# Kernel tuning notes

Measured on AMD Instinct MI355X. Metric: run time of the kernel, lower is better.

## Reference

```python
import jax, jax.numpy as jnp
import numpy as np

ALPHA = 0.5  # leak rate (module default)


def setup_inputs() -> dict:
    key = jax.random.key(0)
    k1, k2, k3 = jax.random.split(key, 3)
    T, nInput, nRes = 4096, 4096, 2048
    x = jax.random.normal(k1, (T, nInput), dtype=jnp.float32)
    # gamma=0.01 scaled input weights, as in the module
    Win = 0.01 * jax.random.normal(k2, (nInput, nRes), dtype=jnp.float32)
    # recurrent weights ~ unit spectral radius (1/sqrt(N) scaling of iid gaussian)
    W = jax.random.normal(k3, (nRes, nRes), dtype=jnp.float32) / jnp.sqrt(nRes)
    return {"x": x, "Win": Win, "W": W}


def reference(x, Win, W):
    # Input projection is time-independent -> hoist out of the recurrence.
    uproj = x @ Win  # [T, nRes]

    def step(v, u):
        v_new = (1.0 - ALPHA) * v + ALPHA * jnp.tanh(v @ W + u)
        return v_new, v_new

    v0 = jnp.zeros((W.shape[0],), dtype=x.dtype)
    _, states = jax.lax.scan(step, v0, uproj)  # states: [T, nRes]
    return states
```

## Files before the change

kernel.cpp:

```cpp
#include <hip/hip_runtime.h>

#define NRES 2048
#define NBLK 256
#define RBUF 4

typedef unsigned long long u64;

__global__ __launch_bounds__(256) void transpose_k(const float* __restrict__ W,
                                                   float* __restrict__ Wt) {
  __shared__ float tile[32][33];
  const int tx = threadIdx.x, ty = threadIdx.y;
  const int x = blockIdx.x * 32 + tx;
  const int y0 = blockIdx.y * 32;
#pragma unroll
  for (int j = ty; j < 32; j += 8)
    tile[j][tx] = W[(size_t)(y0 + j) * NRES + x];
  __syncthreads();
  const int x2 = blockIdx.y * 32 + tx;
  const int y2 = blockIdx.x * 32;
#pragma unroll
  for (int j = ty; j < 32; j += 8)
    Wt[(size_t)(y2 + j) * NRES + x2] = tile[tx][j];
}

__global__ __launch_bounds__(256) void gemm_uproj(const float* __restrict__ X,
                                                  const float* __restrict__ B,
                                                  float* __restrict__ U,
                                                  int M, int N, int K) {
  __shared__ float As[16][128];
  __shared__ float Bs[16][128];
  const int tid = threadIdx.x;
  const int tx = tid & 15, ty = tid >> 4;
  const int m0 = blockIdx.y * 128, n0 = blockIdx.x * 128;

  float acc[8][8];
#pragma unroll
  for (int i = 0; i < 8; i++)
#pragma unroll
    for (int j = 0; j < 8; j++) acc[i][j] = 0.f;

  const int sam = tid >> 1, sak = (tid & 1) * 8;
  const int sbk = tid >> 4, sbn = (tid & 15) * 8;

  for (int k0 = 0; k0 < K; k0 += 16) {
    const float* ap = X + (size_t)(m0 + sam) * K + k0 + sak;
    float4 a0 = *(const float4*)(ap);
    float4 a1 = *(const float4*)(ap + 4);
    As[sak + 0][sam] = a0.x; As[sak + 1][sam] = a0.y;
    As[sak + 2][sam] = a0.z; As[sak + 3][sam] = a0.w;
    As[sak + 4][sam] = a1.x; As[sak + 5][sam] = a1.y;
    As[sak + 6][sam] = a1.z; As[sak + 7][sam] = a1.w;
    const float* bp = B + (size_t)(k0 + sbk) * N + n0 + sbn;
    *(float4*)&Bs[sbk][sbn]     = *(const float4*)(bp);
    *(float4*)&Bs[sbk][sbn + 4] = *(const float4*)(bp + 4);
    __syncthreads();
#pragma unroll
    for (int kk = 0; kk < 16; kk++) {
      float a[8], b[8];
      *(float4*)&a[0] = *(const float4*)&As[kk][ty * 8];
      *(float4*)&a[4] = *(const float4*)&As[kk][ty * 8 + 4];
      *(float4*)&b[0] = *(const float4*)&Bs[kk][tx * 8];
      *(float4*)&b[4] = *(const float4*)&Bs[kk][tx * 8 + 4];
#pragma unroll
      for (int i = 0; i < 8; i++)
#pragma unroll
        for (int j = 0; j < 8; j++) acc[i][j] += a[i] * b[j];
    }
    __syncthreads();
  }
#pragma unroll
  for (int i = 0; i < 8; i++) {
    float* dst = U + (size_t)(m0 + ty * 8 + i) * N + n0 + tx * 8;
    *(float4*)dst       = *(float4*)&acc[i][0];
    *(float4*)(dst + 4) = *(float4*)&acc[i][4];
  }
}

__global__ __launch_bounds__(256, 1) void esn_scan(const float* __restrict__ Wt,
                                                   const float* __restrict__ W,
                                                   u64* vtag,
                                                   float* __restrict__ UY,
                                                   int T) {
  __shared__ float v_lds[2][NRES];
  const int b = blockIdx.x;
  const int tid = threadIdx.x;
  const int wv = tid >> 6;
  const int lane = tid & 63;
  const int h = lane >> 5;
  const int s = lane & 31;
  const int j = b * 8 + wv * 2 + h;

  float2 w2[32];
  if (Wt) {
    const float2* wrow = (const float2*)(Wt + (size_t)j * NRES);
#pragma unroll
    for (int k = 0; k < 32; ++k) w2[k] = wrow[s + 32 * k];
  } else {
#pragma unroll
    for (int k = 0; k < 32; ++k) {
      w2[k].x = W[(size_t)(2 * s + 64 * k) * NRES + j];
      w2[k].y = W[(size_t)(2 * s + 64 * k + 1) * NRES + j];
    }
  }

  float vold = 0.f;

#pragma unroll
  for (int q = 0; q < 8; ++q) v_lds[0][tid + 256 * q] = 0.f;
  __syncthreads();

  for (int t = 0; t < T; ++t) {
    const int buf = t & 1;
    const size_t idx = (size_t)t * NRES + j;
    float u = (s == 0) ? UY[idx] : 0.f;

    if (t > 0) {
      u64* src = vtag + (size_t)((t - 1) & (RBUF - 1)) * NRES;
      unsigned done = 0;
      while (done != 0xFFu) {
        u64 w[8];
#pragma unroll
        for (int q = 0; q < 8; ++q)
          w[q] = __hip_atomic_load(&src[tid + 256 * q], __ATOMIC_RELAXED,
                                   __HIP_MEMORY_SCOPE_AGENT);
#pragma unroll
        for (int q = 0; q < 8; ++q) {
          if (!(done & (1u << q)) && (unsigned)(w[q] >> 32) == (unsigned)t) {
            v_lds[buf][tid + 256 * q] = __uint_as_float((unsigned)w[q]);
            done |= 1u << q;
          }
        }
      }
      __syncthreads();
    }

    float acc0 = 0.f, acc1 = 0.f;
#pragma unroll
    for (int k = 0; k < 32; k += 2) {
      float2 va = *(const float2*)&v_lds[buf][2 * s + 64 * k];
      float2 vb = *(const float2*)&v_lds[buf][2 * s + 64 * (k + 1)];
      acc0 += w2[k].x * va.x + w2[k].y * va.y;
      acc1 += w2[k + 1].x * vb.x + w2[k + 1].y * vb.y;
    }
    float acc = acc0 + acc1;
#pragma unroll
    for (int off = 16; off >= 1; off >>= 1) acc += __shfl_xor(acc, off);

    if (s == 0) {
      float xx = acc + u;
      float e = __expf(2.f * xx);
      float th = 1.f - 2.f / (e + 1.f);
      float vnew = 0.5f * vold + 0.5f * th;
      vold = vnew;
      UY[idx] = vnew;
      u64 w = ((u64)(unsigned)(t + 1) << 32) | (u64)__float_as_uint(vnew);
      (void)__hip_atomic_exchange(&vtag[(size_t)(t & (RBUF - 1)) * NRES + j],
                                  w, __ATOMIC_RELAXED,
                                  __HIP_MEMORY_SCOPE_AGENT);
    }
  }
}

extern "C" void kernel_launch(void* const* d_in, const int* in_sizes, int n_in,
                              void* d_out, int out_size, void* d_ws, size_t ws_size,
                              hipStream_t stream) {
  const float* x   = (const float*)d_in[0];
  const float* Win = (const float*)d_in[1];
  const float* W   = (const float*)d_in[2];
  float* U = (float*)d_out;

  const int T = out_size / NRES;
  const int K = in_sizes[0] / T;

  char* ws = (char*)d_ws;
  u64* vtag = (u64*)ws;
  const size_t vtag_bytes = (size_t)RBUF * NRES * sizeof(u64);
  float* Wt = nullptr;
  const size_t wt_need = vtag_bytes + (size_t)NRES * NRES * sizeof(float);
  if (ws_size >= wt_need) Wt = (float*)(ws + vtag_bytes);

  hipMemsetAsync(vtag, 0, vtag_bytes, stream);

  if (Wt) transpose_k<<<dim3(NRES / 32, NRES / 32), dim3(32, 8), 0, stream>>>(W, Wt);

  gemm_uproj<<<dim3(NRES / 128, T / 128), 256, 0, stream>>>(x, Win, U, T, NRES, K);

  void* args[] = {(void*)&Wt, (void*)&W, (void*)&vtag, (void*)&U, (void*)&T};
  hipLaunchCooperativeKernel((const void*)esn_scan, dim3(NBLK), dim3(256), args,
                             0, stream);
}
```

Before: 14.29 ms.

## Relay recurrent state through per-XCD mirror buffers to cut cross-die polling

Elects one block per XCD (read from the XCC_ID hardware register) as a relay. Only that block polls the global tagged state buffer, and it copies each value it observes into a mirror buffer belonging to its XCD. The other blocks first spin on their local mirror with sc0 loads, which are meant to hit the XCD-local L2, and fall back to global polling after a bounded number of spins. The aim is to cut cross-die coherence traffic and poll latency in the per-step grid sync. In exchange it adds an extra hop of latency through the relay, and it depends on the relay block making progress.

After: 30.01 ms. +110.0%, slower.

```diff
diff --git a/kernel.cpp b/kernel.cpp
--- a/kernel.cpp
+++ b/kernel.cpp
@@ -3,8 +3,11 @@
 #define NRES 2048
 #define NBLK 256
 #define RBUF 4
+#define NXCD 8
+#define MIR_SPINS 16
 
 typedef unsigned long long u64;
+typedef unsigned int u32;
 
 __global__ __launch_bounds__(256) void transpose_k(const float* __restrict__ W,
                                                    float* __restrict__ Wt) {
@@ -79,9 +82,12 @@
 __global__ __launch_bounds__(256, 1) void esn_scan(const float* __restrict__ Wt,
                                                    const float* __restrict__ W,
                                                    u64* vtag,
+                                                   u64* mirror,
+                                                   u32* xcd_cnt,
                                                    float* __restrict__ UY,
-                                                   int T) {
+                                                   int T, int relay_on) {
   __shared__ float v_lds[2][NRES];
+  __shared__ int sh_relay, sh_xcd;
   const int b = blockIdx.x;
   const int tid = threadIdx.x;
   const int wv = tid >> 6;
@@ -90,6 +96,15 @@
   const int s = lane & 31;
   const int j = b * 8 + wv * 2 + h;
 
+  if (tid == 0) {
+    u32 xcc;
+    asm volatile("s_getreg_b32 %0, hwreg(HW_REG_XCC_ID)" : "=s"(xcc));
+    const int mx = (int)(xcc & (NXCD - 1));
+    sh_xcd = mx;
+    int rank = relay_on ? (int)atomicAdd(&xcd_cnt[mx * 16], 1u) : 1;
+    sh_relay = (relay_on && rank == 0) ? 1 : 0;
+  }
+
   float2 w2[32];
   if (Wt) {
     const float2* wrow = (const float2*)(Wt + (size_t)j * NRES);
@@ -104,10 +119,11 @@
   }
 
   float vold = 0.f;
-
 #pragma unroll
   for (int q = 0; q < 8; ++q) v_lds[0][tid + 256 * q] = 0.f;
   __syncthreads();
+  const int myxcd = sh_xcd;
+  const bool polls_global = (sh_relay != 0) || !relay_on;
 
   for (int t = 0; t < T; ++t) {
     const int buf = t & 1;
@@ -115,19 +131,69 @@
     float u = (s == 0) ? UY[idx] : 0.f;
 
     if (t > 0) {
-      u64* src = vtag + (size_t)((t - 1) & (RBUF - 1)) * NRES;
+      const int slot = (t - 1) & (RBUF - 1);
+      u64* src = vtag + (size_t)slot * NRES;
       unsigned done = 0;
-      while (done != 0xFFu) {
-        u64 w[8];
-#pragma unroll
-        for (int q = 0; q < 8; ++q)
-          w[q] = __hip_atomic_load(&src[tid + 256 * q], __ATOMIC_RELAXED,
-                                   __HIP_MEMORY_SCOPE_AGENT);
-#pragma unroll
-        for (int q = 0; q < 8; ++q) {
-          if (!(done & (1u << q)) && (unsigned)(w[q] >> 32) == (unsigned)t) {
-            v_lds[buf][tid + 256 * q] = __uint_as_float((unsigned)w[q]);
-            done |= 1u << q;
+      if (polls_global) {
+        u64* mir = mirror + ((size_t)myxcd * RBUF + slot) * NRES;
+        while (done != 0xFFu) {
+          u64 w[8];
+#pragma unroll
+          for (int q = 0; q < 8; ++q)
+            w[q] = __hip_atomic_load(&src[tid + 256 * q], __ATOMIC_RELAXED,
+                                     __HIP_MEMORY_SCOPE_AGENT);
+#pragma unroll
+          for (int q = 0; q < 8; ++q) {
+            if (!(done & (1u << q)) && (u32)(w[q] >> 32) == (u32)t) {
+              if (relay_on) mir[tid + 256 * q] = w[q];
+              v_lds[buf][tid + 256 * q] = __uint_as_float((u32)w[q]);
+              done |= 1u << q;
+            }
+          }
+        }
+      } else {
+        const u64 mb =
+            (u64)(mirror + ((size_t)myxcd * RBUF + slot) * NRES) + (u64)tid * 8u;
+        for (int spin = 0; done != 0xFFu && spin < MIR_SPINS; ++spin) {
+          u64 w0, w1, w2_, w3, w4, w5, w6, w7;
+          asm volatile(
+              "global_load_dwordx2 %0, %8, off sc0\n\t"
+              "global_load_dwordx2 %1, %9, off sc0\n\t"
+              "global_load_dwordx2 %2, %10, off sc0\n\t"
+              "global_load_dwordx2 %3, %11, off sc0\n\t"
+              "global_load_dwordx2 %4, %12, off sc0\n\t"
+              "global_load_dwordx2 %5, %13, off sc0\n\t"
+              "global_load_dwordx2 %6, %14, off sc0\n\t"
+              "global_load_dwordx2 %7, %15, off sc0\n\t"
+              "s_waitcnt vmcnt(0)"
+              : "=&v"(w0), "=&v"(w1), "=&v"(w2_), "=&v"(w3),
+                "=&v"(w4), "=&v"(w5), "=&v"(w6), "=&v"(w7)
+              : "v"(mb + 0 * 2048u), "v"(mb + 1 * 2048u),
+                "v"(mb + 2 * 2048u), "v"(mb + 3 * 2048u),
+                "v"(mb + 4 * 2048u), "v"(mb + 5 * 2048u),
+                "v"(mb + 6 * 2048u), "v"(mb + 7 * 2048u)
+              : "memory");
+#define ESN_CHK(q, wq)                                              \
+          if (!(done & (1u << q)) && (u32)((wq) >> 32) == (u32)t) { \
+            v_lds[buf][tid + 256 * q] = __uint_as_float((u32)(wq)); \
+            done |= 1u << q;                                        \
+          }
+          ESN_CHK(0, w0) ESN_CHK(1, w1) ESN_CHK(2, w2_) ESN_CHK(3, w3)
+          ESN_CHK(4, w4) ESN_CHK(5, w5) ESN_CHK(6, w6) ESN_CHK(7, w7)
+#undef ESN_CHK
+        }
+        while (done != 0xFFu) {
+          u64 w[8];
+#pragma unroll
+          for (int q = 0; q < 8; ++q)
+            w[q] = __hip_atomic_load(&src[tid + 256 * q], __ATOMIC_RELAXED,
+                                     __HIP_MEMORY_SCOPE_AGENT);
+#pragma unroll
+          for (int q = 0; q < 8; ++q) {
+            if (!(done & (1u << q)) && (u32)(w[q] >> 32) == (u32)t) {
+              v_lds[buf][tid + 256 * q] = __uint_as_float((u32)w[q]);
+              done |= 1u << q;
+            }
           }
         }
       }
@@ -153,7 +219,7 @@
       float vnew = 0.5f * vold + 0.5f * th;
       vold = vnew;
       UY[idx] = vnew;
-      u64 w = ((u64)(unsigned)(t + 1) << 32) | (u64)__float_as_uint(vnew);
+      u64 w = ((u64)(u32)(t + 1) << 32) | (u64)__float_as_uint(vnew);
       (void)__hip_atomic_exchange(&vtag[(size_t)(t & (RBUF - 1)) * NRES + j],
                                   w, __ATOMIC_RELAXED,
                                   __HIP_MEMORY_SCOPE_AGENT);
@@ -173,19 +239,22 @@
   const int K = in_sizes[0] / T;
 
   char* ws = (char*)d_ws;
-  u64* vtag = (u64*)ws;
-  const size_t vtag_bytes = (size_t)RBUF * NRES * sizeof(u64);
+  u64* vtag    = (u64*)ws;
+  u32* xcd_cnt = (u32*)(ws + (64 << 10));
+  u64* mirror  = (u64*)(ws + (128 << 10));
+  int relay_on = ws_size >= (640u << 10) ? 1 : 0;
   float* Wt = nullptr;
-  const size_t wt_need = vtag_bytes + (size_t)NRES * NRES * sizeof(float);
-  if (ws_size >= wt_need) Wt = (float*)(ws + vtag_bytes);
-
-  hipMemsetAsync(vtag, 0, vtag_bytes, stream);
+  if (ws_size >= (1u << 20) + (size_t)NRES * NRES * sizeof(float))
+    Wt = (float*)(ws + (1u << 20));
+
+  hipMemsetAsync(ws, 0, relay_on ? (640u << 10) : (68u << 10), stream);
 
   if (Wt) transpose_k<<<dim3(NRES / 32, NRES / 32), dim3(32, 8), 0, stream>>>(W, Wt);
 
   gemm_uproj<<<dim3(NRES / 128, T / 128), 256, 0, stream>>>(x, Win, U, T, NRES, K);
 
-  void* args[] = {(void*)&Wt, (void*)&W, (void*)&vtag, (void*)&U, (void*)&T};
+  void* args[] = {(void*)&Wt, (void*)&W, (void*)&vtag, (void*)&mirror,
+                  (void*)&xcd_cnt, (void*)&U, (void*)&T, (void*)&relay_on};
   hipLaunchCooperativeKernel((const void*)esn_scan, dim3(NBLK), dim3(256), args,
                              0, stream);
 }
```
